# Optimization experiments

Hardware: AMD Instinct MI355X
Metric: run time of the kernel (lower is better)

The kernel has to match this reference:

```python
import jax, jax.numpy as jnp
import numpy as np
from jax import lax

VOCAB, NUM_CLASSES = 21128, 53
EMB, FILT, K = 128, 128, 3
B, L = 512, 512


def setup_inputs() -> dict:
    key = jax.random.key(0)
    ks = jax.random.split(key, 8)
    char_ids = jax.random.randint(ks[0], (B, L), 0, VOCAB, dtype=jnp.int64 if jax.config.jax_enable_x64 else jnp.int32)
    pos_e1 = jax.random.randint(ks[1], (B,), 0, L - 1, dtype=jnp.int32)
    pos_e2 = jax.random.randint(ks[2], (B,), 0, L - 1, dtype=jnp.int32)
    emb_table = jax.random.normal(ks[3], (VOCAB, EMB), dtype=jnp.float32) * 0.02
    emb_table = emb_table.at[0].set(0.0)  # padding_idx=0
    conv_w = jax.random.normal(ks[4], (FILT, EMB, K), dtype=jnp.float32) * (1.0 / np.sqrt(EMB * K))
    conv_b = jax.random.normal(ks[5], (FILT,), dtype=jnp.float32) * 0.01
    fc_w = jax.random.normal(ks[6], (NUM_CLASSES, FILT * 3), dtype=jnp.float32) * (1.0 / np.sqrt(FILT * 3))
    fc_b = jax.random.normal(ks[7], (NUM_CLASSES,), dtype=jnp.float32) * 0.01
    return {"char_ids": char_ids, "pos_e1": pos_e1, "pos_e2": pos_e2,
            "emb_table": emb_table, "conv_w": conv_w, "conv_b": conv_b,
            "fc_w": fc_w, "fc_b": fc_b}


def reference(char_ids, pos_e1, pos_e2, emb_table, conv_w, conv_b, fc_w, fc_b):
    b, seq = char_ids.shape
    x = emb_table[char_ids]                      # (b, L, E)
    x = jnp.transpose(x, (0, 2, 1))              # (b, E, L)
    conv_out = lax.conv_general_dilated(
        x, conv_w, window_strides=(1,), padding=[(K // 2, K // 2)],
        dimension_numbers=("NCH", "OIH", "NCH"))
    conv_out = jax.nn.relu(conv_out + conv_b[None, :, None])  # (b, F, L)

    # sort + clip entity boundaries, replicate e1==e2 -> e2=e1+1 adjustment
    e1 = jnp.clip(jnp.minimum(pos_e1, pos_e2), 0, seq)
    e2 = jnp.clip(jnp.maximum(pos_e1, pos_e2), 0, seq)
    e2 = jnp.where(e1 == e2, jnp.minimum(e1 + 1, seq), e2)

    idx = jnp.arange(seq)[None, :]               # (1, L)
    m1 = idx < jnp.maximum(e1, 1)[:, None]       # [:e1] or [:1] if e1==0
    m2 = (idx >= e1[:, None]) & (idx < e2[:, None])
    m3 = idx >= jnp.minimum(e2, seq - 1)[:, None]  # [e2:] or last col if e2==L

    neg = jnp.float32(-jnp.inf)
    def seg_max(mask):
        return jnp.max(jnp.where(mask[:, None, :], conv_out, neg), axis=-1)  # (b, F)

    pooled = jnp.concatenate([seg_max(m1), seg_max(m2), seg_max(m3)], axis=-1)  # (b, 3F)
    return pooled @ fc_w.T + fc_b
```

## Files before the change

### kernel.cpp

```cpp
#include <hip/hip_runtime.h>
#include <stdint.h>

#define VOCAB 21128
#define NUMC  53
#define EMB   128
#define SEQ   512
#define BATCH 512

typedef __bf16 bf16x8 __attribute__((ext_vector_type(8)));
typedef float f32x4 __attribute__((ext_vector_type(4)));

__device__ __forceinline__ unsigned int f2bf1(float f) {
    union { float f; unsigned int u; } v; v.f = f;
    return (v.u + 0x7FFFu + ((v.u >> 16) & 1u)) >> 16;
}
__device__ __forceinline__ unsigned int pack2(float a, float b) {
    return f2bf1(a) | (f2bf1(b) << 16);
}

__global__ void prep_kernel(const float* __restrict__ emb, const float* __restrict__ cw,
                            unsigned short* __restrict__ Tb, unsigned short* __restrict__ Wp) {
    int idx = blockIdx.x * blockDim.x + threadIdx.x;
    const int n8 = VOCAB * EMB / 8;
    if (idx < n8) {
        const float4* src = (const float4*)emb + (size_t)idx * 2;
        float4 a = src[0], b = src[1];
        uint4 o;
        o.x = pack2(a.x, a.y);
        o.y = pack2(a.z, a.w);
        o.z = pack2(b.x, b.y);
        o.w = pack2(b.z, b.w);
        *(uint4*)(Tb + (size_t)idx * 8) = o;
    }
    if (idx < 12 * 8 * 64 * 8) {
        int j = idx & 7, l = (idx >> 3) & 63, g = (idx >> 9) & 7, s = idx >> 12;
        int kk = s * 32 + (l >> 4) * 8 + j;
        int f = g * 16 + (l & 15);
        int tap = kk >> 7, e = kk & 127;
        Wp[idx] = (unsigned short)f2bf1(cw[(f * EMB + e) * 3 + tap]);
    }
}

__launch_bounds__(256, 5)
__global__ void pcnn_tile(const int* __restrict__ cid, const int* __restrict__ p1,
                          const int* __restrict__ p2,
                          const unsigned short* __restrict__ Tb,
                          const unsigned short* __restrict__ Wp,
                          float* __restrict__ Pd) {
    __shared__ __align__(16) unsigned short xs[66 * 128];

    const int bx   = blockIdx.x;
    const int b    = bx >> 3;
    const int tq   = bx & 7;
    const int tid  = threadIdx.x;
    const int lane = tid & 63;
    const int wn   = tid >> 6;
    const int quad = lane >> 4;
    const int lc   = lane & 15;

    const int* crow = cid + (size_t)b * SEQ;
    const char* TbB = (const char*)Tb;
    char* xsB = (char*)xs;

    uint4 st[5];
    int   slot[5];
#pragma unroll
    for (int i = 0; i < 5; ++i) {
        int task = tid + 256 * i;
        if (i < 4 || tid < 32) {
            int r = task >> 4, c = task & 15;
            int p = tq * 64 + r - 1;
            unsigned int id = (p >= 0 && p < SEQ) ? (unsigned int)crow[p] : 0u;
            st[i]   = *(const uint4*)(TbB + (size_t)id * 256u + c * 16);
            slot[i] = (r * 16 + (c ^ (r & 15))) * 16;
        }
    }
#pragma unroll
    for (int i = 0; i < 5; ++i) {
        if (i < 4 || tid < 32)
            *(uint4*)(xsB + slot[i]) = st[i];
    }

    int e1 = min(p1[b], p2[b]);
    int e2 = max(p1[b], p2[b]);
    if (e1 == e2) e2 = min(e1 + 1, SEQ);
    const int e1m = max(e1, 1);

    __syncthreads();

    f32x4 acc[4][2];
#pragma unroll
    for (int mt = 0; mt < 4; ++mt)
#pragma unroll
        for (int nt = 0; nt < 2; ++nt)
            acc[mt][nt] = (f32x4){0.f, 0.f, 0.f, 0.f};

#pragma unroll
    for (int s = 0; s < 12; ++s) {
        const int tap = s >> 2;
        const int q   = (s & 3) * 4 + quad;
        const int cs  = q ^ ((lc + tap) & 15);
        bf16x8 b0 = *(const bf16x8*)(Wp + (size_t)((s * 8 + wn * 2) * 64 + lane) * 8);
        bf16x8 b1 = *(const bf16x8*)(Wp + (size_t)((s * 8 + wn * 2 + 1) * 64 + lane) * 8);
#pragma unroll
        for (int mt = 0; mt < 4; ++mt) {
            int r = mt * 16 + lc + tap;
            bf16x8 a = *(const bf16x8*)(xs + r * 128 + cs * 8);
            acc[mt][0] = __builtin_amdgcn_mfma_f32_16x16x32_bf16(a, b0, acc[mt][0], 0, 0, 0);
            acc[mt][1] = __builtin_amdgcn_mfma_f32_16x16x32_bf16(a, b1, acc[mt][1], 0, 0, 0);
        }
    }

    float smax[3][2];
#pragma unroll
    for (int s3 = 0; s3 < 3; ++s3) { smax[s3][0] = -1e30f; smax[s3][1] = -1e30f; }

#pragma unroll
    for (int mt = 0; mt < 4; ++mt)
#pragma unroll
        for (int reg = 0; reg < 4; ++reg) {
            int p = tq * 64 + mt * 16 + quad * 4 + reg;
            float a0 = (p < e1m) ? 0.f : -2e30f;
            float a1 = (p >= e1 && p < e2) ? 0.f : -2e30f;
            float a2 = (p >= e2) ? 0.f : -2e30f;
#pragma unroll
            for (int nt = 0; nt < 2; ++nt) {
                float v = acc[mt][nt][reg];
                smax[0][nt] = fmaxf(smax[0][nt], v + a0);
                smax[1][nt] = fmaxf(smax[1][nt], v + a1);
                smax[2][nt] = fmaxf(smax[2][nt], v + a2);
            }
        }

#pragma unroll
    for (int s3 = 0; s3 < 3; ++s3)
#pragma unroll
        for (int nt = 0; nt < 2; ++nt) {
            float v = smax[s3][nt];
            v = fmaxf(v, __shfl_xor(v, 16));
            v = fmaxf(v, __shfl_xor(v, 32));
            smax[s3][nt] = v;
        }
    if (lane < 16) {
        float* pd = Pd + ((size_t)b * 8 + tq) * 384;
#pragma unroll
        for (int s3 = 0; s3 < 3; ++s3)
#pragma unroll
            for (int nt = 0; nt < 2; ++nt)
                pd[s3 * 128 + wn * 32 + nt * 16 + lc] = smax[s3][nt];
    }
}

__launch_bounds__(256)
__global__ void pcnn_combine(const float* __restrict__ Pd, const float* __restrict__ cb,
                             const float* __restrict__ fcw, const float* __restrict__ fcb,
                             float* __restrict__ out) {
    __shared__ float pooled[384];
    __shared__ float fcred[NUMC][4];
    const int b = blockIdx.x;
    const int tid = threadIdx.x;

    for (int j = tid; j < 384; j += 256) {
        const float* pp = Pd + (size_t)b * 8 * 384 + j;
        float m0 = fmaxf(pp[0 * 384], pp[1 * 384]);
        float m1 = fmaxf(pp[2 * 384], pp[3 * 384]);
        float m2 = fmaxf(pp[4 * 384], pp[5 * 384]);
        float m3 = fmaxf(pp[6 * 384], pp[7 * 384]);
        float m = fmaxf(fmaxf(m0, m1), fmaxf(m2, m3));
        pooled[j] = fmaxf(m + cb[j & 127], 0.f);
    }
    __syncthreads();

    if (tid < 212) {
        int c = tid >> 2, q = tid & 3;
        const float* wrow = fcw + (size_t)c * 384 + q * 96;
        const float* pp   = pooled + q * 96;
        float sum = 0.f;
#pragma unroll 8
        for (int i = 0; i < 96; ++i) sum += wrow[i] * pp[i];
        fcred[c][q] = sum;
    }
    __syncthreads();
    if (tid < NUMC)
        out[(size_t)b * NUMC + tid] =
            fcred[tid][0] + fcred[tid][1] + fcred[tid][2] + fcred[tid][3] + fcb[tid];
}

extern "C" void kernel_launch(void* const* d_in, const int* in_sizes, int n_in,
                              void* d_out, int out_size, void* d_ws, size_t ws_size,
                              hipStream_t stream) {
    const int*   cid = (const int*)d_in[0];
    const int*   p1  = (const int*)d_in[1];
    const int*   p2  = (const int*)d_in[2];
    const float* emb = (const float*)d_in[3];
    const float* cw  = (const float*)d_in[4];
    const float* cb  = (const float*)d_in[5];
    const float* fcw = (const float*)d_in[6];
    const float* fcb = (const float*)d_in[7];
    float* out = (float*)d_out;

    unsigned short* Tb = (unsigned short*)d_ws;
    unsigned short* Wp = (unsigned short*)((char*)d_ws + (size_t)VOCAB * EMB * 2);
    float*          Pd = (float*)((char*)d_ws + (size_t)VOCAB * EMB * 2 + 98304);

    const int n8 = VOCAB * EMB / 8;
    const int prep_threads = 256;
    const int prep_blocks  = (n8 + prep_threads - 1) / prep_threads;
    prep_kernel<<<prep_blocks, prep_threads, 0, stream>>>(emb, cw, Tb, Wp);
    pcnn_tile<<<BATCH * 8, 256, 0, stream>>>(cid, p1, p2, Tb, Wp, Pd);
    pcnn_combine<<<BATCH, 256, 0, stream>>>(Pd, cb, fcw, fcb, out);
}
```

Measured before the change: 129.2 us.

## Process two 64-row chunks per block with double-buffered LDS prefetch

```diff
diff --git a/kernel.cpp b/kernel.cpp
--- a/kernel.cpp
+++ b/kernel.cpp
@@ -41,17 +41,17 @@
     }
 }
 
-__launch_bounds__(256, 5)
+__launch_bounds__(256, 4)
 __global__ void pcnn_tile(const int* __restrict__ cid, const int* __restrict__ p1,
                           const int* __restrict__ p2,
                           const unsigned short* __restrict__ Tb,
                           const unsigned short* __restrict__ Wp,
                           float* __restrict__ Pd) {
-    __shared__ __align__(16) unsigned short xs[66 * 128];
+    __shared__ __align__(16) unsigned short xs[2][66 * 128];
 
     const int bx   = blockIdx.x;
-    const int b    = bx >> 3;
-    const int tq   = bx & 7;
+    const int b    = bx >> 2;
+    const int th   = bx & 3;
     const int tid  = threadIdx.x;
     const int lane = tid & 63;
     const int wn   = tid >> 6;
@@ -60,77 +60,96 @@
 
     const int* crow = cid + (size_t)b * SEQ;
     const char* TbB = (const char*)Tb;
-    char* xsB = (char*)xs;
-
-    uint4 st[5];
-    int   slot[5];
-#pragma unroll
-    for (int i = 0; i < 5; ++i) {
-        int task = tid + 256 * i;
-        if (i < 4 || tid < 32) {
-            int r = task >> 4, c = task & 15;
-            int p = tq * 64 + r - 1;
-            unsigned int id = (p >= 0 && p < SEQ) ? (unsigned int)crow[p] : 0u;
-            st[i]   = *(const uint4*)(TbB + (size_t)id * 256u + c * 16);
-            slot[i] = (r * 16 + (c ^ (r & 15))) * 16;
-        }
-    }
-#pragma unroll
-    for (int i = 0; i < 5; ++i) {
-        if (i < 4 || tid < 32)
-            *(uint4*)(xsB + slot[i]) = st[i];
-    }
 
     int e1 = min(p1[b], p2[b]);
     int e2 = max(p1[b], p2[b]);
     if (e1 == e2) e2 = min(e1 + 1, SEQ);
     const int e1m = max(e1, 1);
 
-    __syncthreads();
-
-    f32x4 acc[4][2];
-#pragma unroll
-    for (int mt = 0; mt < 4; ++mt)
-#pragma unroll
-        for (int nt = 0; nt < 2; ++nt)
-            acc[mt][nt] = (f32x4){0.f, 0.f, 0.f, 0.f};
-
-#pragma unroll
-    for (int s = 0; s < 12; ++s) {
-        const int tap = s >> 2;
-        const int q   = (s & 3) * 4 + quad;
-        const int cs  = q ^ ((lc + tap) & 15);
-        bf16x8 b0 = *(const bf16x8*)(Wp + (size_t)((s * 8 + wn * 2) * 64 + lane) * 8);
-        bf16x8 b1 = *(const bf16x8*)(Wp + (size_t)((s * 8 + wn * 2 + 1) * 64 + lane) * 8);
-#pragma unroll
-        for (int mt = 0; mt < 4; ++mt) {
-            int r = mt * 16 + lc + tap;
-            bf16x8 a = *(const bf16x8*)(xs + r * 128 + cs * 8);
-            acc[mt][0] = __builtin_amdgcn_mfma_f32_16x16x32_bf16(a, b0, acc[mt][0], 0, 0, 0);
-            acc[mt][1] = __builtin_amdgcn_mfma_f32_16x16x32_bf16(a, b1, acc[mt][1], 0, 0, 0);
-        }
-    }
-
-    float smax[3][2];
-#pragma unroll
-    for (int s3 = 0; s3 < 3; ++s3) { smax[s3][0] = -1e30f; smax[s3][1] = -1e30f; }
-
-#pragma unroll
-    for (int mt = 0; mt < 4; ++mt)
-#pragma unroll
-        for (int reg = 0; reg < 4; ++reg) {
-            int p = tq * 64 + mt * 16 + quad * 4 + reg;
-            float a0 = (p < e1m) ? 0.f : -2e30f;
-            float a1 = (p >= e1 && p < e2) ? 0.f : -2e30f;
-            float a2 = (p >= e2) ? 0.f : -2e30f;
-#pragma unroll
-            for (int nt = 0; nt < 2; ++nt) {
-                float v = acc[mt][nt][reg];
-                smax[0][nt] = fmaxf(smax[0][nt], v + a0);
-                smax[1][nt] = fmaxf(smax[1][nt], v + a1);
-                smax[2][nt] = fmaxf(smax[2][nt], v + a2);
+    uint4 st[5];
+    int   slot[5];
+    auto LOAD = [&](int half) {
+#pragma unroll
+        for (int i = 0; i < 5; ++i) {
+            int task = tid + 256 * i;
+            if (i < 4 || tid < 32) {
+                int r = task >> 4, c = task & 15;
+                int p = th * 128 + half * 64 + r - 1;
+                unsigned int id = (p >= 0 && p < SEQ) ? (unsigned int)crow[p] : 0u;
+                st[i]   = *(const uint4*)(TbB + (size_t)id * 256u + c * 16);
+                slot[i] = (r * 16 + (c ^ (r & 15))) * 16;
             }
         }
+    };
+    auto WRITE = [&](int buf) {
+        char* dst = (char*)xs[buf];
+#pragma unroll
+        for (int i = 0; i < 5; ++i)
+            if (i < 4 || tid < 32)
+                *(uint4*)(dst + slot[i]) = st[i];
+    };
+
+    float smax[3][2];
+#pragma unroll
+    for (int s3 = 0; s3 < 3; ++s3) { smax[s3][0] = -1e30f; smax[s3][1] = -1e30f; }
+
+    auto COMPUTE = [&](const unsigned short* xsc, int pbase) {
+        f32x4 acc[4][2];
+#pragma unroll
+        for (int mt = 0; mt < 4; ++mt)
+#pragma unroll
+            for (int nt = 0; nt < 2; ++nt)
+                acc[mt][nt] = (f32x4){0.f, 0.f, 0.f, 0.f};
+
+#pragma unroll
+        for (int s = 0; s < 12; ++s) {
+            const int tap = s >> 2;
+            const int q   = (s & 3) * 4 + quad;
+            const int cs  = q ^ ((lc + tap) & 15);
+            bf16x8 b0 = *(const bf16x8*)(Wp + (size_t)((s * 8 + wn * 2) * 64 + lane) * 8);
+            bf16x8 b1 = *(const bf16x8*)(Wp + (size_t)((s * 8 + wn * 2 + 1) * 64 + lane) * 8);
+#pragma unroll
+            for (int mt = 0; mt < 4; ++mt) {
+                int r = mt * 16 + lc + tap;
+                bf16x8 a = *(const bf16x8*)(xsc + r * 128 + cs * 8);
+                acc[mt][0] = __builtin_amdgcn_mfma_f32_16x16x32_bf16(a, b0, acc[mt][0], 0, 0, 0);
+                acc[mt][1] = __builtin_amdgcn_mfma_f32_16x16x32_bf16(a, b1, acc[mt][1], 0, 0, 0);
+            }
+        }
+
+#pragma unroll
+        for (int mt = 0; mt < 4; ++mt)
+#pragma unroll
+            for (int reg = 0; reg < 4; ++reg) {
+                int p = pbase + mt * 16 + quad * 4 + reg;
+                float a0 = (p < e1m) ? 0.f : -2e30f;
+                float a1 = (p >= e1 && p < e2) ? 0.f : -2e30f;
+                float a2 = (p >= e2) ? 0.f : -2e30f;
+#pragma unroll
+                for (int nt = 0; nt < 2; ++nt) {
+                    float v = acc[mt][nt][reg];
+                    smax[0][nt] = fmaxf(smax[0][nt], v + a0);
+                    smax[1][nt] = fmaxf(smax[1][nt], v + a1);
+                    smax[2][nt] = fmaxf(smax[2][nt], v + a2);
+                }
+            }
+    };
+
+    LOAD(0);
+    WRITE(0);
+    asm volatile("s_waitcnt lgkmcnt(0)" ::: "memory");
+    __builtin_amdgcn_s_barrier();
+
+    LOAD(1);
+    __builtin_amdgcn_sched_barrier(0);
+
+    COMPUTE(xs[0], th * 128);
+
+    WRITE(1);
+    asm volatile("s_waitcnt lgkmcnt(0)" ::: "memory");
+    __builtin_amdgcn_s_barrier();
+
+    COMPUTE(xs[1], th * 128 + 64);
 
 #pragma unroll
     for (int s3 = 0; s3 < 3; ++s3)
@@ -142,7 +161,7 @@
             smax[s3][nt] = v;
         }
     if (lane < 16) {
-        float* pd = Pd + ((size_t)b * 8 + tq) * 384;
+        float* pd = Pd + ((size_t)b * 4 + th) * 384;
 #pragma unroll
         for (int s3 = 0; s3 < 3; ++s3)
 #pragma unroll
@@ -161,12 +180,8 @@
     const int tid = threadIdx.x;
 
     for (int j = tid; j < 384; j += 256) {
-        const float* pp = Pd + (size_t)b * 8 * 384 + j;
-        float m0 = fmaxf(pp[0 * 384], pp[1 * 384]);
-        float m1 = fmaxf(pp[2 * 384], pp[3 * 384]);
-        float m2 = fmaxf(pp[4 * 384], pp[5 * 384]);
-        float m3 = fmaxf(pp[6 * 384], pp[7 * 384]);
-        float m = fmaxf(fmaxf(m0, m1), fmaxf(m2, m3));
+        const float* pp = Pd + (size_t)b * 4 * 384 + j;
+        float m = fmaxf(fmaxf(pp[0], pp[384]), fmaxf(pp[768], pp[1152]));
         pooled[j] = fmaxf(m + cb[j & 127], 0.f);
     }
     __syncthreads();
@@ -207,6 +222,6 @@
     const int prep_threads = 256;
     const int prep_blocks  = (n8 + prep_threads - 1) / prep_threads;
     prep_kernel<<<prep_blocks, prep_threads, 0, stream>>>(emb, cw, Tb, Wp);
-    pcnn_tile<<<BATCH * 8, 256, 0, stream>>>(cid, p1, p2, Tb, Wp, Pd);
+    pcnn_tile<<<BATCH * 4, 256, 0, stream>>>(cid, p1, p2, Tb, Wp, Pd);
     pcnn_combine<<<BATCH, 256, 0, stream>>>(Pd, cb, fcw, fcb, out);
 }
```

Result: no change. 128.8 us (-0.4%).
